# Performance work log

Hardware: AMD Instinct MI355X
Metric: run time of the kernel (lower is better)

The kernel has to match this reference:

```python
import jax, jax.numpy as jnp
import numpy as np

LOGIT_TEMP = 0.1
EPS = 1e-8


def _compute_logits(px, tgt, emb):
    # px: [F, D] selected projected frames; tgt: [F] int labels; emb: [C, D]
    pxn = px / jnp.maximum(jnp.linalg.norm(px, axis=-1, keepdims=True), EPS)
    embn = emb / jnp.maximum(jnp.linalg.norm(emb, axis=-1, keepdims=True), EPS)
    pos = jnp.sum(pxn * embn[tgt], axis=-1)          # [F] cosine to positive
    neg = jnp.einsum('fd,cd->fc', pxn, embn)          # [F, C] cosine to all classes
    # neg_is_pos: emb row of target exactly equals the neg row (torch: (pos==negs).all(-1))
    row_eq = jnp.all(emb[:, None, :] == emb[None, :, :], axis=-1)  # [C, C]
    neg_is_pos = row_eq[:, tgt].T                     # [F, C]
    neg = jnp.where(neg_is_pos, -jnp.inf, neg / LOGIT_TEMP)
    return jnp.concatenate([pos[:, None] / LOGIT_TEMP, neg], axis=1)  # [F, C+1]


def setup_inputs() -> dict:
    key = jax.random.key(0)
    k = jax.random.split(key, 7)
    B, T, De, Df, C = 16, 1500, 768, 256, 500
    n_m = n_u = 12000
    x = jax.random.normal(k[0], (B, T, De), dtype=jnp.float32)
    label = jax.random.randint(k[1], (B, T), 0, C, dtype=jnp.int32)
    mask_m = jax.random.randint(k[2], (n_m,), 0, B * T, dtype=jnp.int32)
    mask_u = jax.random.randint(k[3], (n_u,), 0, B * T, dtype=jnp.int32)
    W = jax.random.normal(k[4], (De, Df), dtype=jnp.float32) * 0.02
    b = jnp.zeros((Df,), dtype=jnp.float32)
    emb = jax.random.uniform(k[5], (C, Df), dtype=jnp.float32)  # torch uniform_ init
    return {"x": x, "label": label, "mask_m": mask_m, "mask_u": mask_u,
            "W": W, "b": b, "emb": emb}


def reference(x, label, mask_m, mask_u, W, b, emb):
    proj = jnp.einsum('bte,ef->btf', x, W) + b        # final_proj
    Df = proj.shape[-1]
    pf = proj.reshape(-1, Df)                          # [B*T, Df]
    lf = label.reshape(-1)
    logit_m = _compute_logits(pf[mask_m], lf[mask_m], emb)
    logit_u = _compute_logits(pf[mask_u], lf[mask_u], emb)
    return (logit_m, logit_u)
```

## Files before the change

### kernel.cpp

```cpp
#include <hip/hip_runtime.h>
#include <math.h>

typedef unsigned short u16;
typedef unsigned int   u32;
typedef __attribute__((ext_vector_type(4))) float          f32x4;
typedef __attribute__((ext_vector_type(8))) short          short8;
typedef __attribute__((ext_vector_type(4))) unsigned int   u32x4;
typedef __attribute__((ext_vector_type(8))) unsigned short u16x8;

#define NSEL   24000
#define NHALF  12000
#define D_E    768
#define D_F    256
#define NC     500
#define NCP    512
#define MASK_VAL -3.0e38f

__device__ inline u16 f2bf(float f) {
    u32 u = __float_as_uint(f);
    return (u16)((u + 0x7FFFu + ((u >> 16) & 1u)) >> 16);
}

__device__ inline u32 pack2(float lo, float hi) {
    return (u32)f2bf(lo) | ((u32)f2bf(hi) << 16);
}

__device__ inline short8 pack8(const float4 lo, const float4 hi) {
    u32x4 w;
    w.x = pack2(lo.x, lo.y);
    w.y = pack2(lo.z, lo.w);
    w.z = pack2(hi.x, hi.y);
    w.w = pack2(hi.z, hi.w);
    return __builtin_bit_cast(short8, w);
}

__global__ void prep_w(const float* __restrict__ W, u16* __restrict__ Wt) {
    __shared__ float tile[32][33];
    const int k0 = blockIdx.x * 32, n0 = blockIdx.y * 32;
    const int tx = threadIdx.x, ty = threadIdx.y;
    #pragma unroll
    for (int i = 0; i < 4; ++i)
        tile[ty + i * 8][tx] = W[(size_t)(k0 + ty + i * 8) * D_F + n0 + tx];
    __syncthreads();
    #pragma unroll
    for (int i = 0; i < 4; ++i)
        Wt[(size_t)(n0 + ty + i * 8) * D_E + k0 + tx] = f2bf(tile[tx][ty + i * 8]);
}

__global__ void prep_emb(const float* __restrict__ emb, u16* __restrict__ Et) {
    const int c = blockIdx.x, t = threadIdx.x;
    if (c >= NC) { Et[(size_t)c * D_F + t] = 0; return; }
    const float v = emb[(size_t)c * D_F + t];
    float sq = v * v;
    #pragma unroll
    for (int o = 32; o > 0; o >>= 1) sq += __shfl_xor(sq, o);
    __shared__ float ws2[4];
    if ((t & 63) == 0) ws2[t >> 6] = sq;
    __syncthreads();
    const float tot = ws2[0] + ws2[1] + ws2[2] + ws2[3];
    const float inv = 1.0f / fmaxf(sqrtf(tot), 1e-8f);
    Et[(size_t)c * D_F + t] = f2bf(v * inv);
}

__global__ void eqcls_kernel(const float* __restrict__ emb, u16* __restrict__ eqcls) {
    const int c = blockIdx.x;
    if (c >= NC) { if (threadIdx.x == 0) eqcls[c] = 0xFFFFu; return; }
    const int t = threadIdx.x;
    int best = c;
    const float4* ra = (const float4*)(emb + (size_t)c * D_F);
    for (int d = t; d < c; d += 256) {
        const float4* rb = (const float4*)(emb + (size_t)d * D_F);
        bool eq = true;
        for (int k = 0; k < D_F / 4; ++k) {
            const float4 a = ra[k], bq = rb[k];
            if (a.x != bq.x || a.y != bq.y || a.z != bq.z || a.w != bq.w) { eq = false; break; }
        }
        if (eq) best = min(best, d);
    }
    #pragma unroll
    for (int o = 32; o > 0; o >>= 1) best = min(best, __shfl_xor(best, o));
    __shared__ int red[4];
    if ((t & 63) == 0) red[t >> 6] = best;
    __syncthreads();
    if (t == 0) eqcls[c] = (u16)min(min(red[0], red[1]), min(red[2], red[3]));
}

__global__ __launch_bounds__(256, 4)
void proj_mfma(const float* __restrict__ x, const u16* __restrict__ Wt,
               const float* __restrict__ b, u16* __restrict__ pxnb) {
    const int tid  = threadIdx.x;
    const int lane = tid & 63, wid = tid >> 6;
    const int lg   = lane >> 4, l15 = lane & 15;
    const int row0 = blockIdx.x * 32;

    const float* xa0 = x + (size_t)(row0 + l15)      * D_E + lg * 8;
    const float* xa1 = x + (size_t)(row0 + 16 + l15) * D_E + lg * 8;
    const u16* wb0 = Wt + (size_t)(wid * 64 +  0 + l15) * D_E + lg * 8;
    const u16* wb1 = Wt + (size_t)(wid * 64 + 16 + l15) * D_E + lg * 8;
    const u16* wb2 = Wt + (size_t)(wid * 64 + 32 + l15) * D_E + lg * 8;
    const u16* wb3 = Wt + (size_t)(wid * 64 + 48 + l15) * D_E + lg * 8;

    f32x4 acc[2][4] = {};

    #pragma unroll 4
    for (int kt = 0; kt < D_E / 32; ++kt) {
        const int k0 = kt * 32;
        const float4 a0l = *(const float4*)(xa0 + k0);
        const float4 a0h = *(const float4*)(xa0 + k0 + 4);
        const float4 a1l = *(const float4*)(xa1 + k0);
        const float4 a1h = *(const float4*)(xa1 + k0 + 4);
        const short8 a0 = pack8(a0l, a0h);
        const short8 a1 = pack8(a1l, a1h);
        const short8 b0 = __builtin_bit_cast(short8, *(const u16x8*)(wb0 + k0));
        const short8 b1 = __builtin_bit_cast(short8, *(const u16x8*)(wb1 + k0));
        const short8 b2 = __builtin_bit_cast(short8, *(const u16x8*)(wb2 + k0));
        const short8 b3 = __builtin_bit_cast(short8, *(const u16x8*)(wb3 + k0));
        acc[0][0] = __builtin_amdgcn_mfma_f32_16x16x32_bf16(a0, b0, acc[0][0], 0, 0, 0);
        acc[0][1] = __builtin_amdgcn_mfma_f32_16x16x32_bf16(a0, b1, acc[0][1], 0, 0, 0);
        acc[0][2] = __builtin_amdgcn_mfma_f32_16x16x32_bf16(a0, b2, acc[0][2], 0, 0, 0);
        acc[0][3] = __builtin_amdgcn_mfma_f32_16x16x32_bf16(a0, b3, acc[0][3], 0, 0, 0);
        acc[1][0] = __builtin_amdgcn_mfma_f32_16x16x32_bf16(a1, b0, acc[1][0], 0, 0, 0);
        acc[1][1] = __builtin_amdgcn_mfma_f32_16x16x32_bf16(a1, b1, acc[1][1], 0, 0, 0);
        acc[1][2] = __builtin_amdgcn_mfma_f32_16x16x32_bf16(a1, b2, acc[1][2], 0, 0, 0);
        acc[1][3] = __builtin_amdgcn_mfma_f32_16x16x32_bf16(a1, b3, acc[1][3], 0, 0, 0);
    }

    __shared__ float sq[32];
    if (tid < 32) sq[tid] = 0.0f;
    __syncthreads();

    float bb[4];
    #pragma unroll
    for (int n = 0; n < 4; ++n) bb[n] = b[wid * 64 + n * 16 + l15];
    #pragma unroll
    for (int m = 0; m < 2; ++m)
        #pragma unroll
        for (int n = 0; n < 4; ++n)
            #pragma unroll
            for (int q = 0; q < 4; ++q) acc[m][n][q] += bb[n];

    #pragma unroll
    for (int m = 0; m < 2; ++m)
        #pragma unroll
        for (int q = 0; q < 4; ++q) {
            float p = 0.0f;
            #pragma unroll
            for (int n = 0; n < 4; ++n) p += acc[m][n][q] * acc[m][n][q];
            p += __shfl_xor(p, 1); p += __shfl_xor(p, 2);
            p += __shfl_xor(p, 4); p += __shfl_xor(p, 8);
            if (l15 == 0) atomicAdd(&sq[m * 16 + lg * 4 + q], p);
        }
    __syncthreads();

    #pragma unroll
    for (int m = 0; m < 2; ++m)
        #pragma unroll
        for (int q = 0; q < 4; ++q) {
            const int row = m * 16 + lg * 4 + q;
            const float inv = 1.0f / fmaxf(sqrtf(sq[row]), 1e-8f);
            #pragma unroll
            for (int n = 0; n < 4; ++n) {
                const int col = wid * 64 + n * 16 + l15;
                pxnb[(size_t)(row0 + row) * D_F + col] = f2bf(acc[m][n][q] * inv);
            }
        }
}

__global__ __launch_bounds__(256, 4)
void logits_mfma(const u16* __restrict__ pxnb, const u16* __restrict__ Et,
                 const u16* __restrict__ eqcls_g, const int* __restrict__ label,
                 const int* __restrict__ mm, const int* __restrict__ mu,
                 float* __restrict__ out) {
    __shared__ int sel_s[32];
    __shared__ int tgt_s[32];
    __shared__ u16 tcls_s[32];
    __shared__ u16 ecls_s[256];
    const int tid  = threadIdx.x;
    const int lane = tid & 63, wid = tid >> 6;
    const int lg   = lane >> 4, l15 = lane & 15;
    const int row0 = blockIdx.x * 32;
    const int nb   = blockIdx.y * 256;

    if (tid < 32) {
        const int i   = row0 + tid;
        const int sel = (i < NHALF) ? mm[i] : mu[i - NHALF];
        sel_s[tid] = sel;
        const int tg = label[sel];
        tgt_s[tid]  = tg;
        tcls_s[tid] = eqcls_g[tg];
    }
    ecls_s[tid] = eqcls_g[nb + tid];
    __syncthreads();

    const u16* pa0 = pxnb + (size_t)sel_s[l15]      * D_F + lg * 8;
    const u16* pa1 = pxnb + (size_t)sel_s[16 + l15] * D_F + lg * 8;
    const u16* eb0 = Et + (size_t)(nb + wid * 64 +  0 + l15) * D_F + lg * 8;
    const u16* eb1 = Et + (size_t)(nb + wid * 64 + 16 + l15) * D_F + lg * 8;
    const u16* eb2 = Et + (size_t)(nb + wid * 64 + 32 + l15) * D_F + lg * 8;
    const u16* eb3 = Et + (size_t)(nb + wid * 64 + 48 + l15) * D_F + lg * 8;

    f32x4 acc[2][4] = {};

    #pragma unroll
    for (int kt = 0; kt < D_F / 32; ++kt) {
        const int k0 = kt * 32;
        const short8 a0 = __builtin_bit_cast(short8, *(const u16x8*)(pa0 + k0));
        const short8 a1 = __builtin_bit_cast(short8, *(const u16x8*)(pa1 + k0));
        const short8 b0 = __builtin_bit_cast(short8, *(const u16x8*)(eb0 + k0));
        const short8 b1 = __builtin_bit_cast(short8, *(const u16x8*)(eb1 + k0));
        const short8 b2 = __builtin_bit_cast(short8, *(const u16x8*)(eb2 + k0));
        const short8 b3 = __builtin_bit_cast(short8, *(const u16x8*)(eb3 + k0));
        acc[0][0] = __builtin_amdgcn_mfma_f32_16x16x32_bf16(a0, b0, acc[0][0], 0, 0, 0);
        acc[0][1] = __builtin_amdgcn_mfma_f32_16x16x32_bf16(a0, b1, acc[0][1], 0, 0, 0);
        acc[0][2] = __builtin_amdgcn_mfma_f32_16x16x32_bf16(a0, b2, acc[0][2], 0, 0, 0);
        acc[0][3] = __builtin_amdgcn_mfma_f32_16x16x32_bf16(a0, b3, acc[0][3], 0, 0, 0);
        acc[1][0] = __builtin_amdgcn_mfma_f32_16x16x32_bf16(a1, b0, acc[1][0], 0, 0, 0);
        acc[1][1] = __builtin_amdgcn_mfma_f32_16x16x32_bf16(a1, b1, acc[1][1], 0, 0, 0);
        acc[1][2] = __builtin_amdgcn_mfma_f32_16x16x32_bf16(a1, b2, acc[1][2], 0, 0, 0);
        acc[1][3] = __builtin_amdgcn_mfma_f32_16x16x32_bf16(a1, b3, acc[1][3], 0, 0, 0);
    }

    #pragma unroll
    for (int m = 0; m < 2; ++m)
        #pragma unroll
        for (int q = 0; q < 4; ++q) {
            const int rloc = m * 16 + lg * 4 + q;
            const int i    = row0 + rloc;
            const u16 tc   = tcls_s[rloc];
            const int tg   = tgt_s[rloc];
            float* orow    = out + (size_t)i * (NC + 1);
            #pragma unroll
            for (int n = 0; n < 4; ++n) {
                const int col16 = wid * 64 + n * 16 + l15;
                const int c     = nb + col16;
                if (c < NC) {
                    const float val = acc[m][n][q] * 10.0f;
                    orow[1 + c] = (ecls_s[col16] == tc) ? MASK_VAL : val;
                    if (c == tg) orow[0] = val;
                }
            }
        }
}

extern "C" void kernel_launch(void* const* d_in, const int* in_sizes, int n_in,
                              void* d_out, int out_size, void* d_ws, size_t ws_size,
                              hipStream_t stream) {
    const float* x     = (const float*)d_in[0];
    const int*   label = (const int*)  d_in[1];
    const int*   mm    = (const int*)  d_in[2];
    const int*   mu    = (const int*)  d_in[3];
    const float* W     = (const float*)d_in[4];
    const float* b     = (const float*)d_in[5];
    const float* emb   = (const float*)d_in[6];
    float* out = (float*)d_out;

    u16* pxnb = (u16*)d_ws;
    u16* Wt   = pxnb + (size_t)NSEL * D_F;
    u16* Et   = Wt + (size_t)D_F * D_E;
    u16* eqc  = Et + (size_t)NCP * D_F;

    prep_w      <<<dim3(D_E / 32, D_F / 32), dim3(32, 8), 0, stream>>>(W, Wt);
    prep_emb    <<<NCP, 256, 0, stream>>>(emb, Et);
    eqcls_kernel<<<NCP, 256, 0, stream>>>(emb, eqc);
    proj_mfma   <<<NSEL / 32, 256, 0, stream>>>(x, Wt, b, pxnb);
    logits_mfma <<<dim3(NSEL / 32, 2), 256, 0, stream>>>(pxnb, Et, eqc, label, mm, mu, out);
}
```

Before: 227.3 us.

## Halve row tile to 16 and register-prefetch next K-step in both GEMMs

Both the projection and logits kernels now process 16 rows per block instead of 32, which doubles the grid and halves the per-thread accumulator count. Each K-loop also loads the next step's A and B fragments into registers before issuing the current MFMAs, a software double-buffer meant to hide global-load latency. The cost is that each block reuses the W and embedding fragments over half as many rows, so more redundant weight reads go through cache. The smaller tile is also meant to spread work more evenly across CUs and raise occupancy.

```diff
diff --git a/kernel.cpp b/kernel.cpp
--- a/kernel.cpp
+++ b/kernel.cpp
@@ -91,79 +91,76 @@
     const int tid  = threadIdx.x;
     const int lane = tid & 63, wid = tid >> 6;
     const int lg   = lane >> 4, l15 = lane & 15;
-    const int row0 = blockIdx.x * 32;
-
-    const float* xa0 = x + (size_t)(row0 + l15)      * D_E + lg * 8;
-    const float* xa1 = x + (size_t)(row0 + 16 + l15) * D_E + lg * 8;
-    const u16* wb0 = Wt + (size_t)(wid * 64 +  0 + l15) * D_E + lg * 8;
-    const u16* wb1 = Wt + (size_t)(wid * 64 + 16 + l15) * D_E + lg * 8;
-    const u16* wb2 = Wt + (size_t)(wid * 64 + 32 + l15) * D_E + lg * 8;
-    const u16* wb3 = Wt + (size_t)(wid * 64 + 48 + l15) * D_E + lg * 8;
-
-    f32x4 acc[2][4] = {};
-
-    #pragma unroll 4
+    const int row0 = blockIdx.x * 16;
+
+    const float* xa  = x  + (size_t)(row0 + l15) * D_E + lg * 8;
+    const u16*   wb0 = Wt + (size_t)(wid * 64 +  0 + l15) * D_E + lg * 8;
+    const u16*   wb1 = Wt + (size_t)(wid * 64 + 16 + l15) * D_E + lg * 8;
+    const u16*   wb2 = Wt + (size_t)(wid * 64 + 32 + l15) * D_E + lg * 8;
+    const u16*   wb3 = Wt + (size_t)(wid * 64 + 48 + l15) * D_E + lg * 8;
+
+    f32x4 acc[4] = {};
+
+    float4 nAl = *(const float4*)(xa);
+    float4 nAh = *(const float4*)(xa + 4);
+    u16x8  nB0 = *(const u16x8*)(wb0);
+    u16x8  nB1 = *(const u16x8*)(wb1);
+    u16x8  nB2 = *(const u16x8*)(wb2);
+    u16x8  nB3 = *(const u16x8*)(wb3);
+
+    #pragma unroll
     for (int kt = 0; kt < D_E / 32; ++kt) {
-        const int k0 = kt * 32;
-        const float4 a0l = *(const float4*)(xa0 + k0);
-        const float4 a0h = *(const float4*)(xa0 + k0 + 4);
-        const float4 a1l = *(const float4*)(xa1 + k0);
-        const float4 a1h = *(const float4*)(xa1 + k0 + 4);
-        const short8 a0 = pack8(a0l, a0h);
-        const short8 a1 = pack8(a1l, a1h);
-        const short8 b0 = __builtin_bit_cast(short8, *(const u16x8*)(wb0 + k0));
-        const short8 b1 = __builtin_bit_cast(short8, *(const u16x8*)(wb1 + k0));
-        const short8 b2 = __builtin_bit_cast(short8, *(const u16x8*)(wb2 + k0));
-        const short8 b3 = __builtin_bit_cast(short8, *(const u16x8*)(wb3 + k0));
-        acc[0][0] = __builtin_amdgcn_mfma_f32_16x16x32_bf16(a0, b0, acc[0][0], 0, 0, 0);
-        acc[0][1] = __builtin_amdgcn_mfma_f32_16x16x32_bf16(a0, b1, acc[0][1], 0, 0, 0);
-        acc[0][2] = __builtin_amdgcn_mfma_f32_16x16x32_bf16(a0, b2, acc[0][2], 0, 0, 0);
-        acc[0][3] = __builtin_amdgcn_mfma_f32_16x16x32_bf16(a0, b3, acc[0][3], 0, 0, 0);
-        acc[1][0] = __builtin_amdgcn_mfma_f32_16x16x32_bf16(a1, b0, acc[1][0], 0, 0, 0);
-        acc[1][1] = __builtin_amdgcn_mfma_f32_16x16x32_bf16(a1, b1, acc[1][1], 0, 0, 0);
-        acc[1][2] = __builtin_amdgcn_mfma_f32_16x16x32_bf16(a1, b2, acc[1][2], 0, 0, 0);
-        acc[1][3] = __builtin_amdgcn_mfma_f32_16x16x32_bf16(a1, b3, acc[1][3], 0, 0, 0);
-    }
-
-    __shared__ float sq[32];
-    if (tid < 32) sq[tid] = 0.0f;
+        const float4 cAl = nAl, cAh = nAh;
+        const u16x8  cB0 = nB0, cB1 = nB1, cB2 = nB2, cB3 = nB3;
+        if (kt + 1 < D_E / 32) {
+            const int k1 = (kt + 1) * 32;
+            nAl = *(const float4*)(xa + k1);
+            nAh = *(const float4*)(xa + k1 + 4);
+            nB0 = *(const u16x8*)(wb0 + k1);
+            nB1 = *(const u16x8*)(wb1 + k1);
+            nB2 = *(const u16x8*)(wb2 + k1);
+            nB3 = *(const u16x8*)(wb3 + k1);
+        }
+        const short8 a = pack8(cAl, cAh);
+        acc[0] = __builtin_amdgcn_mfma_f32_16x16x32_bf16(a, __builtin_bit_cast(short8, cB0), acc[0], 0, 0, 0);
+        acc[1] = __builtin_amdgcn_mfma_f32_16x16x32_bf16(a, __builtin_bit_cast(short8, cB1), acc[1], 0, 0, 0);
+        acc[2] = __builtin_amdgcn_mfma_f32_16x16x32_bf16(a, __builtin_bit_cast(short8, cB2), acc[2], 0, 0, 0);
+        acc[3] = __builtin_amdgcn_mfma_f32_16x16x32_bf16(a, __builtin_bit_cast(short8, cB3), acc[3], 0, 0, 0);
+    }
+
+    __shared__ float sq[16];
+    if (tid < 16) sq[tid] = 0.0f;
     __syncthreads();
 
     float bb[4];
     #pragma unroll
     for (int n = 0; n < 4; ++n) bb[n] = b[wid * 64 + n * 16 + l15];
     #pragma unroll
-    for (int m = 0; m < 2; ++m)
-        #pragma unroll
-        for (int n = 0; n < 4; ++n)
-            #pragma unroll
-            for (int q = 0; q < 4; ++q) acc[m][n][q] += bb[n];
-
-    #pragma unroll
-    for (int m = 0; m < 2; ++m)
-        #pragma unroll
-        for (int q = 0; q < 4; ++q) {
-            float p = 0.0f;
-            #pragma unroll
-            for (int n = 0; n < 4; ++n) p += acc[m][n][q] * acc[m][n][q];
-            p += __shfl_xor(p, 1); p += __shfl_xor(p, 2);
-            p += __shfl_xor(p, 4); p += __shfl_xor(p, 8);
-            if (l15 == 0) atomicAdd(&sq[m * 16 + lg * 4 + q], p);
-        }
-    __syncthreads();
-
-    #pragma unroll
-    for (int m = 0; m < 2; ++m)
-        #pragma unroll
-        for (int q = 0; q < 4; ++q) {
-            const int row = m * 16 + lg * 4 + q;
-            const float inv = 1.0f / fmaxf(sqrtf(sq[row]), 1e-8f);
-            #pragma unroll
-            for (int n = 0; n < 4; ++n) {
-                const int col = wid * 64 + n * 16 + l15;
-                pxnb[(size_t)(row0 + row) * D_F + col] = f2bf(acc[m][n][q] * inv);
-            }
-        }
+    for (int n = 0; n < 4; ++n)
+        #pragma unroll
+        for (int q = 0; q < 4; ++q) acc[n][q] += bb[n];
+
+    #pragma unroll
+    for (int q = 0; q < 4; ++q) {
+        float p = 0.0f;
+        #pragma unroll
+        for (int n = 0; n < 4; ++n) p += acc[n][q] * acc[n][q];
+        p += __shfl_xor(p, 1); p += __shfl_xor(p, 2);
+        p += __shfl_xor(p, 4); p += __shfl_xor(p, 8);
+        if (l15 == 0) atomicAdd(&sq[lg * 4 + q], p);
+    }
+    __syncthreads();
+
+    #pragma unroll
+    for (int q = 0; q < 4; ++q) {
+        const int row = lg * 4 + q;
+        const float inv = 1.0f / fmaxf(sqrtf(sq[row]), 1e-8f);
+        #pragma unroll
+        for (int n = 0; n < 4; ++n) {
+            const int col = wid * 64 + n * 16 + l15;
+            pxnb[(size_t)(row0 + row) * D_F + col] = f2bf(acc[n][q] * inv);
+        }
+    }
 }
 
 __global__ __launch_bounds__(256, 4)
@@ -171,17 +168,17 @@
                  const u16* __restrict__ eqcls_g, const int* __restrict__ label,
                  const int* __restrict__ mm, const int* __restrict__ mu,
                  float* __restrict__ out) {
-    __shared__ int sel_s[32];
-    __shared__ int tgt_s[32];
-    __shared__ u16 tcls_s[32];
+    __shared__ int sel_s[16];
+    __shared__ int tgt_s[16];
+    __shared__ u16 tcls_s[16];
     __shared__ u16 ecls_s[256];
     const int tid  = threadIdx.x;
     const int lane = tid & 63, wid = tid >> 6;
     const int lg   = lane >> 4, l15 = lane & 15;
-    const int row0 = blockIdx.x * 32;
+    const int row0 = blockIdx.x * 16;
     const int nb   = blockIdx.y * 256;
 
-    if (tid < 32) {
+    if (tid < 16) {
         const int i   = row0 + tid;
         const int sel = (i < NHALF) ? mm[i] : mu[i - NHALF];
         sel_s[tid] = sel;
@@ -192,54 +189,56 @@
     ecls_s[tid] = eqcls_g[nb + tid];
     __syncthreads();
 
-    const u16* pa0 = pxnb + (size_t)sel_s[l15]      * D_F + lg * 8;
-    const u16* pa1 = pxnb + (size_t)sel_s[16 + l15] * D_F + lg * 8;
+    const u16* pa  = pxnb + (size_t)sel_s[l15] * D_F + lg * 8;
     const u16* eb0 = Et + (size_t)(nb + wid * 64 +  0 + l15) * D_F + lg * 8;
     const u16* eb1 = Et + (size_t)(nb + wid * 64 + 16 + l15) * D_F + lg * 8;
     const u16* eb2 = Et + (size_t)(nb + wid * 64 + 32 + l15) * D_F + lg * 8;
     const u16* eb3 = Et + (size_t)(nb + wid * 64 + 48 + l15) * D_F + lg * 8;
 
-    f32x4 acc[2][4] = {};
+    f32x4 acc[4] = {};
+
+    u16x8 nA  = *(const u16x8*)(pa);
+    u16x8 nB0 = *(const u16x8*)(eb0);
+    u16x8 nB1 = *(const u16x8*)(eb1);
+    u16x8 nB2 = *(const u16x8*)(eb2);
+    u16x8 nB3 = *(const u16x8*)(eb3);
 
     #pragma unroll
     for (int kt = 0; kt < D_F / 32; ++kt) {
-        const int k0 = kt * 32;
-        const short8 a0 = __builtin_bit_cast(short8, *(const u16x8*)(pa0 + k0));
-        const short8 a1 = __builtin_bit_cast(short8, *(const u16x8*)(pa1 + k0));
-        const short8 b0 = __builtin_bit_cast(short8, *(const u16x8*)(eb0 + k0));
-        const short8 b1 = __builtin_bit_cast(short8, *(const u16x8*)(eb1 + k0));
-        const short8 b2 = __builtin_bit_cast(short8, *(const u16x8*)(eb2 + k0));
-        const short8 b3 = __builtin_bit_cast(short8, *(const u16x8*)(eb3 + k0));
-        acc[0][0] = __builtin_amdgcn_mfma_f32_16x16x32_bf16(a0, b0, acc[0][0], 0, 0, 0);
-        acc[0][1] = __builtin_amdgcn_mfma_f32_16x16x32_bf16(a0, b1, acc[0][1], 0, 0, 0);
-        acc[0][2] = __builtin_amdgcn_mfma_f32_16x16x32_bf16(a0, b2, acc[0][2], 0, 0, 0);
-        acc[0][3] = __builtin_amdgcn_mfma_f32_16x16x32_bf16(a0, b3, acc[0][3], 0, 0, 0);
-        acc[1][0] = __builtin_amdgcn_mfma_f32_16x16x32_bf16(a1, b0, acc[1][0], 0, 0, 0);
-        acc[1][1] = __builtin_amdgcn_mfma_f32_16x16x32_bf16(a1, b1, acc[1][1], 0, 0, 0);
-        acc[1][2] = __builtin_amdgcn_mfma_f32_16x16x32_bf16(a1, b2, acc[1][2], 0, 0, 0);
-        acc[1][3] = __builtin_amdgcn_mfma_f32_16x16x32_bf16(a1, b3, acc[1][3], 0, 0, 0);
-    }
-
-    #pragma unroll
-    for (int m = 0; m < 2; ++m)
-        #pragma unroll
-        for (int q = 0; q < 4; ++q) {
-            const int rloc = m * 16 + lg * 4 + q;
-            const int i    = row0 + rloc;
-            const u16 tc   = tcls_s[rloc];
-            const int tg   = tgt_s[rloc];
-            float* orow    = out + (size_t)i * (NC + 1);
-            #pragma unroll
-            for (int n = 0; n < 4; ++n) {
-                const int col16 = wid * 64 + n * 16 + l15;
-                const int c     = nb + col16;
-                if (c < NC) {
-                    const float val = acc[m][n][q] * 10.0f;
-                    orow[1 + c] = (ecls_s[col16] == tc) ? MASK_VAL : val;
-                    if (c == tg) orow[0] = val;
-                }
+        const u16x8 cA = nA, cB0 = nB0, cB1 = nB1, cB2 = nB2, cB3 = nB3;
+        if (kt + 1 < D_F / 32) {
+            const int k1 = (kt + 1) * 32;
+            nA  = *(const u16x8*)(pa  + k1);
+            nB0 = *(const u16x8*)(eb0 + k1);
+            nB1 = *(const u16x8*)(eb1 + k1);
+            nB2 = *(const u16x8*)(eb2 + k1);
+            nB3 = *(const u16x8*)(eb3 + k1);
+        }
+        const short8 a = __builtin_bit_cast(short8, cA);
+        acc[0] = __builtin_amdgcn_mfma_f32_16x16x32_bf16(a, __builtin_bit_cast(short8, cB0), acc[0], 0, 0, 0);
+        acc[1] = __builtin_amdgcn_mfma_f32_16x16x32_bf16(a, __builtin_bit_cast(short8, cB1), acc[1], 0, 0, 0);
+        acc[2] = __builtin_amdgcn_mfma_f32_16x16x32_bf16(a, __builtin_bit_cast(short8, cB2), acc[2], 0, 0, 0);
+        acc[3] = __builtin_amdgcn_mfma_f32_16x16x32_bf16(a, __builtin_bit_cast(short8, cB3), acc[3], 0, 0, 0);
+    }
+
+    #pragma unroll
+    for (int q = 0; q < 4; ++q) {
+        const int rloc = lg * 4 + q;
+        const int i    = row0 + rloc;
+        const u16 tc   = tcls_s[rloc];
+        const int tg   = tgt_s[rloc];
+        float* orow    = out + (size_t)i * (NC + 1);
+        #pragma unroll
+        for (int n = 0; n < 4; ++n) {
+            const int col16 = wid * 64 + n * 16 + l15;
+            const int c     = nb + col16;
+            if (c < NC) {
+                const float val = acc[n][q] * 10.0f;
+                orow[1 + c] = (ecls_s[col16] == tc) ? MASK_VAL : val;
+                if (c == tg) orow[0] = val;
             }
         }
+    }
 }
 
 extern "C" void kernel_launch(void* const* d_in, const int* in_sizes, int n_in,
@@ -262,6 +261,6 @@
     prep_w      <<<dim3(D_E / 32, D_F / 32), dim3(32, 8), 0, stream>>>(W, Wt);
     prep_emb    <<<NCP, 256, 0, stream>>>(emb, Et);
     eqcls_kernel<<<NCP, 256, 0, stream>>>(emb, eqc);
-    proj_mfma   <<<NSEL / 32, 256, 0, stream>>>(x, Wt, b, pxnb);
-    logits_mfma <<<dim3(NSEL / 32, 2), 256, 0, stream>>>(pxnb, Et, eqc, label, mm, mu, out);
-}
+    proj_mfma   <<<NSEL / 16, 256, 0, stream>>>(x, Wt, b, pxnb);
+    logits_mfma <<<dim3(NSEL / 16, 2), 256, 0, stream>>>(pxnb, Et, eqc, label, mm, mu, out);
+}
```

New measurement: 278.4 us. 1.23x slower.
